# Optimization experiments

Measured on AMD Instinct MI355X. Metric: run time of the kernel, lower is better.

The kernel has to match this reference:

```python
import jax, jax.numpy as jnp
import numpy as np

N_ITERS = 1000
LR = 2e-05
ORDER = 16
EPS = 1e-8


def pz_to_sos(sos):
    # sos: (1, ORDER, 6) raw params -> stabilized biquad coefficients
    g = sos[:, :, 0] + 1.0
    pr, pi = sos[:, :, 1], sos[:, :, 2]
    zr, zi = sos[:, :, 3], sos[:, :, 4]
    pabs = jnp.sqrt(pr * pr + pi * pi)
    pscale = jnp.tanh(pabs) / pabs          # pole = pole * tanh(|pole|)/|pole|
    pr, pi = pr * pscale, pi * pscale
    zabs = jnp.sqrt(zr * zr + zi * zi)
    zscale = jnp.tanh(zabs) / zabs
    zr, zi = zr * zscale, zi * zscale
    b0 = g
    b1 = -2.0 * g * zr
    b2 = g * (zr * zr + zi * zi)
    a0 = jnp.ones_like(g)
    a1 = -2.0 * pr
    a2 = pr * pr + pi * pi
    return jnp.stack([b0, b1, b2, a0, a1, a2], axis=-1)  # (1, ORDER, 6)


def sos_log_mag(out_sos, n_freq):
    # Evaluate cascade frequency response at n_freq points on [0, pi]
    w = jnp.linspace(0.0, np.pi, n_freq)                 # (F,)
    e1 = jnp.exp(-1j * w)                                # e^{-jw}, complex64
    e2 = e1 * e1                                         # e^{-2jw}
    b = out_sos[..., :3].astype(jnp.complex64)           # (1, ORDER, 3)
    a = out_sos[..., 3:].astype(jnp.complex64)
    B = b[..., 0:1] + b[..., 1:2] * e1 + b[..., 2:3] * e2  # (1, ORDER, F)
    A = a[..., 0:1] + a[..., 1:2] * e1 + a[..., 2:3] * e2
    h = jnp.prod(B / A, axis=1)                          # (1, F)
    return 20.0 * jnp.log10(jnp.abs(h) + EPS)            # log-magnitude in dB


def run_sgd(target_dB):
    tgt = target_dB.reshape(1, -1)
    n_freq = tgt.shape[-1]

    def loss_fn(sos):
        out = pz_to_sos(sos)
        dB = sos_log_mag(out, n_freq)
        return jnp.mean((dB - tgt) ** 2), out

    def step(sos, _):
        (_, out), g = jax.value_and_grad(loss_fn, has_aux=True)(sos)
        return sos - LR * g, out

    sos0 = jnp.ones((1, ORDER, 6), dtype=target_dB.dtype)
    _, outs = jax.lax.scan(step, sos0, None, length=N_ITERS)
    # torch loop returns out_sos computed from sos BEFORE the final SGD step
    return outs[-1]


def setup_inputs():
    key = jax.random.key(0)
    # target magnitude response in dB (~6 dB scale, EQ-like)
    return {"target_dB": jax.random.normal(key, (512,), dtype=jnp.float32) * 6.0}


def reference(target_dB):
    return run_sgd(target_dB)
```

## Files before the change

### kernel.cpp

```cpp
#include <hip/hip_runtime.h>
#include <math.h>


typedef float v2 __attribute__((ext_vector_type(2)));

#define LRK8_ 3.2683916458e-5f
#define INVK8_ 0.020762050593046017f

__device__ __forceinline__ float rcp_(float x)  { return __builtin_amdgcn_rcpf(x); }
__device__ __forceinline__ float sqrt_(float x) { return __builtin_amdgcn_sqrtf(x); }
__device__ __forceinline__ float log2_(float x) { return __builtin_amdgcn_logf(x); }
__device__ __forceinline__ float exp2_(float x) { return __builtin_amdgcn_exp2f(x); }

template <int CTRL>
__device__ __forceinline__ float dpp_add(float x) {
    int y = __builtin_amdgcn_update_dpp(0, __float_as_int(x), CTRL, 0xF, 0xF, true);
    return x + __int_as_float(y);
}

__device__ __forceinline__ float wave_sum_at63(float x) {
    x = dpp_add<0x111>(x);
    x = dpp_add<0x112>(x);
    x = dpp_add<0x114>(x);
    x = dpp_add<0x118>(x);
    x = dpp_add<0x142>(x);
    x = dpp_add<0x143>(x);
    return x;
}

__device__ __forceinline__ float readlane_f(float x, int l) {
    return __int_as_float(__builtin_amdgcn_readlane(__float_as_int(x), l));
}

__global__ __launch_bounds__(256) void sgd_filter_kernel(const float* __restrict__ tgt,
                                                         float* __restrict__ out) {
    const int tid  = threadIdx.x;
    const int lane = tid & 63;
    const int wv   = tid >> 6;

    const float wA = (float)(3.14159265358979323846 * (double)tid / 511.0);
    const float wB = (float)(3.14159265358979323846 * (double)(tid + 256) / 511.0);
    float s1a, c1a, s1b, c1b;
    sincosf(wA, &s1a, &c1a);
    sincosf(wB, &s1b, &c1b);
    const v2 C1 = {c1a, c1b};
    const v2 S1 = {s1a, s1b};
    const v2 C2 = {c1a * c1a - s1a * s1a, c1b * c1b - s1b * s1b};
    const v2 S2 = {2.0f * c1a * s1a, 2.0f * c1b * s1b};
    const v2 TK8 = {tgt[tid] * INVK8_, tgt[tid + 256] * INVK8_};

    float q0 = 1.0f;
    v2 qr = {1.0f, 1.0f};
    v2 qi = {1.0f, 1.0f};

    __shared__ float part[2][32];

    const int widx = wv << 3;
    const int ridx = (((lane & 3) << 3) | (lane >> 2)) & 31;

    for (int it = 0; it < 999; ++it) {
        float g = q0 + 1.0f;
        v2 d2 = qr * qr + qi * qi;
        v2 u  = {sqrt_(d2.x), sqrt_(d2.y)};
        v2 iu = {rcp_(u.x), rcp_(u.y)};
        v2 ea = u * 2.8853900817779268f;
        v2 e  = {exp2_(ea.x), exp2_(ea.y)};
        v2 e1 = e + 1.0f;
        v2 re = {rcp_(e1.x), rcp_(e1.y)};
        v2 t  = 1.0f - 2.0f * re;
        v2 sc = t * iu;
        v2 rs = qr * sc;
        v2 is = qi * sc;

        float zq = t.y * t.y;
        float b0 = g;
        float b1 = -2.0f * g * rs.y;
        float b2 = g * zq;
        float a1 = -2.0f * rs.x;
        float a2 = t.x * t.x;

        v2 Br = b0 + b1 * C1 + b2 * C2;
        v2 Bi = -(b1 * S1 + b2 * S2);
        v2 Ar = 1.0f + a1 * C1 + a2 * C2;
        v2 Ai = -(a1 * S1 + a2 * S2);
        v2 nb = Br * Br + Bi * Bi;
        v2 na = Ar * Ar + Ai * Ai;
        v2 rnb = {rcp_(nb.x), rcp_(nb.y)};
        v2 rna = {rcp_(na.x), rcp_(na.y)};
        v2 pr = nb * rna;
        v2 lg = {log2_(pr.x), log2_(pr.y)};
        v2 cF = LRK8_ * (lg - TK8);
        v2 cb = cF * rnb;
        v2 ca = cF * rna;
        v2 cbBr = cb * Br, cbBi = cb * Bi;
        v2 caAr = ca * Ar, caAi = ca * Ai;
        v2 gb1v = cbBr * C1 - cbBi * S1;
        v2 gb2v = cbBr * C2 - cbBi * S2;
        v2 ga1v = caAr * C1 - caAi * S1;
        v2 ga2v = caAr * C2 - caAi * S2;

        float t0 = wave_sum_at63(cbBr.x + cbBr.y);
        float t1 = wave_sum_at63(gb1v.x + gb1v.y);
        float t2 = wave_sum_at63(gb2v.x + gb2v.y);
        float t3 = wave_sum_at63(-(ga1v.x + ga1v.y));
        float t4 = wave_sum_at63(-(ga2v.x + ga2v.y));

        const int pp = it & 1;
        if (lane == 63) {
            float* pb = &part[pp][widx];
            pb[0] = t0; pb[1] = t1; pb[2] = t2; pb[3] = t3; pb[4] = t4;
        }
        __syncthreads();

        float y = part[pp][ridx];
        y = dpp_add<0x111>(y);
        y = dpp_add<0x112>(y);
        float S0 = readlane_f(y, 3);
        float Sb1 = readlane_f(y, 7);
        float Sb2 = readlane_f(y, 11);
        float Sa1 = readlane_f(y, 15);
        float Sa2 = readlane_f(y, 19);

        float dg = S0 - 2.0f * rs.y * Sb1 + zq * Sb2;
        v2 gg2 = {2.0f, 2.0f * g};
        v2 S42 = {Sa2, Sb2};
        v2 S31 = {Sa1, Sb1};
        v2 dr = gg2 * (rs * S42 - S31);
        v2 di = gg2 * (is * S42);
        v2 ds = ((1.0f - t * t) - t * iu) * iu;
        v2 dotv = qr * dr + qi * di;
        v2 com = ds * iu * dotv;
        v2 gqr = sc * dr + qr * com;
        v2 gqi = sc * di + qi * com;

        q0 -= dg;
        qr -= gqr;
        qi -= gqi;
    }

    {
        float g = q0 + 1.0f;
        v2 d2 = qr * qr + qi * qi;
        v2 u  = {sqrt_(d2.x), sqrt_(d2.y)};
        v2 iu = {rcp_(u.x), rcp_(u.y)};
        v2 ea = u * 2.8853900817779268f;
        v2 e  = {exp2_(ea.x), exp2_(ea.y)};
        v2 e1 = e + 1.0f;
        v2 re = {rcp_(e1.x), rcp_(e1.y)};
        v2 t  = 1.0f - 2.0f * re;
        v2 sc = t * iu;
        v2 rs = qr * sc;
        float b0 = g;
        float b1 = -2.0f * g * rs.y;
        float b2 = g * (t.y * t.y);
        float a1 = -2.0f * rs.x;
        float a2 = t.x * t.x;
        if (tid < 96) {
            int c = tid % 6;
            float v = (c == 0) ? b0 : (c == 1) ? b1 : (c == 2) ? b2
                    : (c == 3) ? 1.0f : (c == 4) ? a1 : a2;
            out[tid] = v;
        }
    }
}

extern "C" void kernel_launch(void* const* d_in, const int* in_sizes, int n_in,
                              void* d_out, int out_size, void* d_ws, size_t ws_size,
                              hipStream_t stream) {
    (void)in_sizes; (void)n_in; (void)d_ws; (void)ws_size; (void)out_size;
    const float* tgt = (const float*)d_in[0];
    float* out = (float*)d_out;
    hipLaunchKernelGGL(sgd_filter_kernel, dim3(1), dim3(256), 0, stream, tgt, out);
}
```

Before: 473.5 us.

## Collapse block to a single wavefront and drop LDS barrier reduction

The kernel now launches a single 64-lane wavefront instead of four. Each lane handles eight frequency points, held in unrolled register arrays, and accumulates the gradient partials locally before one wave-level DPP reduction per term plus a readlane broadcast. This removes the per-iteration shared-memory write, the __syncthreads and the cross-wave combine. In exchange, all frequency work that used to be spread over four SIMDs now runs serially on one, so each iteration issues about four times as many instructions and raises register pressure.

After: 663.0 us. 40.0% more time.

```diff
diff --git a/kernel.cpp b/kernel.cpp
--- a/kernel.cpp
+++ b/kernel.cpp
@@ -28,35 +28,34 @@
     return x;
 }
 
-__device__ __forceinline__ float readlane_f(float x, int l) {
-    return __int_as_float(__builtin_amdgcn_readlane(__float_as_int(x), l));
+__device__ __forceinline__ float bcast63(float x) {
+    return __int_as_float(__builtin_amdgcn_readlane(__float_as_int(x), 63));
 }
 
-__global__ __launch_bounds__(256) void sgd_filter_kernel(const float* __restrict__ tgt,
-                                                         float* __restrict__ out) {
-    const int tid  = threadIdx.x;
-    const int lane = tid & 63;
-    const int wv   = tid >> 6;
+__global__ __launch_bounds__(64) void sgd_filter_kernel(const float* __restrict__ tgt,
+                                                        float* __restrict__ out) {
+    const int lane = threadIdx.x;
 
-    const float wA = (float)(3.14159265358979323846 * (double)tid / 511.0);
-    const float wB = (float)(3.14159265358979323846 * (double)(tid + 256) / 511.0);
-    float s1a, c1a, s1b, c1b;
-    sincosf(wA, &s1a, &c1a);
-    sincosf(wB, &s1b, &c1b);
-    const v2 C1 = {c1a, c1b};
-    const v2 S1 = {s1a, s1b};
-    const v2 C2 = {c1a * c1a - s1a * s1a, c1b * c1b - s1b * s1b};
-    const v2 S2 = {2.0f * c1a * s1a, 2.0f * c1b * s1b};
-    const v2 TK8 = {tgt[tid] * INVK8_, tgt[tid + 256] * INVK8_};
+    v2 C1[4], S1[4], C2[4], S2[4], TK[4];
+    #pragma unroll
+    for (int j = 0; j < 4; ++j) {
+        int f0 = lane + 64 * j;
+        int f1 = f0 + 256;
+        float wa = (float)(3.14159265358979323846 * (double)f0 / 511.0);
+        float wb = (float)(3.14159265358979323846 * (double)f1 / 511.0);
+        float sa, ca, sb, cb;
+        sincosf(wa, &sa, &ca);
+        sincosf(wb, &sb, &cb);
+        C1[j] = (v2){ca, cb};
+        S1[j] = (v2){sa, sb};
+        C2[j] = (v2){ca * ca - sa * sa, cb * cb - sb * sb};
+        S2[j] = (v2){2.0f * ca * sa, 2.0f * cb * sb};
+        TK[j] = (v2){tgt[f0] * INVK8_, tgt[f1] * INVK8_};
+    }
 
     float q0 = 1.0f;
     v2 qr = {1.0f, 1.0f};
     v2 qi = {1.0f, 1.0f};
-
-    __shared__ float part[2][32];
-
-    const int widx = wv << 3;
-    const int ridx = (((lane & 3) << 3) | (lane >> 2)) & 31;
 
     for (int it = 0; it < 999; ++it) {
         float g = q0 + 1.0f;
@@ -79,47 +78,37 @@
         float a1 = -2.0f * rs.x;
         float a2 = t.x * t.x;
 
-        v2 Br = b0 + b1 * C1 + b2 * C2;
-        v2 Bi = -(b1 * S1 + b2 * S2);
-        v2 Ar = 1.0f + a1 * C1 + a2 * C2;
-        v2 Ai = -(a1 * S1 + a2 * S2);
-        v2 nb = Br * Br + Bi * Bi;
-        v2 na = Ar * Ar + Ai * Ai;
-        v2 rnb = {rcp_(nb.x), rcp_(nb.y)};
-        v2 rna = {rcp_(na.x), rcp_(na.y)};
-        v2 pr = nb * rna;
-        v2 lg = {log2_(pr.x), log2_(pr.y)};
-        v2 cF = LRK8_ * (lg - TK8);
-        v2 cb = cF * rnb;
-        v2 ca = cF * rna;
-        v2 cbBr = cb * Br, cbBi = cb * Bi;
-        v2 caAr = ca * Ar, caAi = ca * Ai;
-        v2 gb1v = cbBr * C1 - cbBi * S1;
-        v2 gb2v = cbBr * C2 - cbBi * S2;
-        v2 ga1v = caAr * C1 - caAi * S1;
-        v2 ga2v = caAr * C2 - caAi * S2;
+        v2 A0 = {0.0f, 0.0f}, A1 = {0.0f, 0.0f}, A2 = {0.0f, 0.0f};
+        v2 A3 = {0.0f, 0.0f}, A4 = {0.0f, 0.0f};
+        #pragma unroll
+        for (int j = 0; j < 4; ++j) {
+            v2 Br = b0 + b1 * C1[j] + b2 * C2[j];
+            v2 Bi = -(b1 * S1[j] + b2 * S2[j]);
+            v2 Ar = 1.0f + a1 * C1[j] + a2 * C2[j];
+            v2 Ai = -(a1 * S1[j] + a2 * S2[j]);
+            v2 nb = Br * Br + Bi * Bi;
+            v2 na = Ar * Ar + Ai * Ai;
+            v2 rnb = {rcp_(nb.x), rcp_(nb.y)};
+            v2 rna = {rcp_(na.x), rcp_(na.y)};
+            v2 r  = nb * rna;
+            v2 lg = {log2_(r.x), log2_(r.y)};
+            v2 cF = LRK8_ * (lg - TK[j]);
+            v2 cb = cF * rnb;
+            v2 ca = cF * rna;
+            v2 cbBr = cb * Br, cbBi = cb * Bi;
+            v2 caAr = ca * Ar, caAi = ca * Ai;
+            A0 += cbBr;
+            A1 += cbBr * C1[j] - cbBi * S1[j];
+            A2 += cbBr * C2[j] - cbBi * S2[j];
+            A3 += caAr * C1[j] - caAi * S1[j];
+            A4 += caAr * C2[j] - caAi * S2[j];
+        }
 
-        float t0 = wave_sum_at63(cbBr.x + cbBr.y);
-        float t1 = wave_sum_at63(gb1v.x + gb1v.y);
-        float t2 = wave_sum_at63(gb2v.x + gb2v.y);
-        float t3 = wave_sum_at63(-(ga1v.x + ga1v.y));
-        float t4 = wave_sum_at63(-(ga2v.x + ga2v.y));
-
-        const int pp = it & 1;
-        if (lane == 63) {
-            float* pb = &part[pp][widx];
-            pb[0] = t0; pb[1] = t1; pb[2] = t2; pb[3] = t3; pb[4] = t4;
-        }
-        __syncthreads();
-
-        float y = part[pp][ridx];
-        y = dpp_add<0x111>(y);
-        y = dpp_add<0x112>(y);
-        float S0 = readlane_f(y, 3);
-        float Sb1 = readlane_f(y, 7);
-        float Sb2 = readlane_f(y, 11);
-        float Sa1 = readlane_f(y, 15);
-        float Sa2 = readlane_f(y, 19);
+        float S0  = bcast63(wave_sum_at63(A0.x + A0.y));
+        float Sb1 = bcast63(wave_sum_at63(A1.x + A1.y));
+        float Sb2 = bcast63(wave_sum_at63(A2.x + A2.y));
+        float Sa1 = bcast63(wave_sum_at63(-(A3.x + A3.y)));
+        float Sa2 = bcast63(wave_sum_at63(-(A4.x + A4.y)));
 
         float dg = S0 - 2.0f * rs.y * Sb1 + zq * Sb2;
         v2 gg2 = {2.0f, 2.0f * g};
@@ -155,11 +144,16 @@
         float b2 = g * (t.y * t.y);
         float a1 = -2.0f * rs.x;
         float a2 = t.x * t.x;
-        if (tid < 96) {
-            int c = tid % 6;
-            float v = (c == 0) ? b0 : (c == 1) ? b1 : (c == 2) ? b2
-                    : (c == 3) ? 1.0f : (c == 4) ? a1 : a2;
-            out[tid] = v;
+
+        int c = lane % 6;
+        float v = (c == 0) ? b0 : (c == 1) ? b1 : (c == 2) ? b2
+                : (c == 3) ? 1.0f : (c == 4) ? a1 : a2;
+        out[lane] = v;
+        if (lane < 32) {
+            int c2 = (lane + 64) % 6;
+            float v2s = (c2 == 0) ? b0 : (c2 == 1) ? b1 : (c2 == 2) ? b2
+                      : (c2 == 3) ? 1.0f : (c2 == 4) ? a1 : a2;
+            out[lane + 64] = v2s;
         }
     }
 }
@@ -170,5 +164,5 @@
     (void)in_sizes; (void)n_in; (void)d_ws; (void)ws_size; (void)out_size;
     const float* tgt = (const float*)d_in[0];
     float* out = (float*)d_out;
-    hipLaunchKernelGGL(sgd_filter_kernel, dim3(1), dim3(256), 0, stream, tgt, out);
+    hipLaunchKernelGGL(sgd_filter_kernel, dim3(1), dim3(64), 0, stream, tgt, out);
 }
```
